# Kernel optimization log

Hardware: AMD Instinct MI355X
Metric: run time of the kernel (lower is better)

## Reference

```python
import jax, jax.numpy as jnp
import numpy as np

TEMPERATURE = 0.05
EPS_NORM = 1e-12  # F.normalize eps
EPS_DEN = 1e-6


def _l2norm_c(x):
    # F.normalize(x, dim=1): x / max(||x||_2, eps)
    n = jnp.sqrt(jnp.sum(x * x, axis=1, keepdims=True))
    return x / jnp.maximum(n, EPS_NORM)


def setup_inputs() -> dict:
    key = jax.random.key(0)
    k1, k2, k3, k4 = jax.random.split(key, 4)
    N, C, H, W = 4, 256, 64, 64
    return {
        "rgb_map": jax.random.normal(k1, (N, C, H, W), dtype=jnp.float32),
        "ir_map": jax.random.normal(k2, (N, C, H, W), dtype=jnp.float32),
        "rgb_mask": jax.random.randint(k3, (N, H, W), 0, 5, dtype=jnp.int64 if jax.config.jax_enable_x64 else jnp.int32),
        "ir_mask": jax.random.randint(k4, (N, H, W), 0, 5, dtype=jnp.int64 if jax.config.jax_enable_x64 else jnp.int32),
    }


def reference(rgb_map, ir_map, rgb_mask, ir_mask):
    N, C, H, W = rgb_map.shape
    HW = H * W
    rgb = _l2norm_c(rgb_map).reshape(N, C, HW)  # (N,C,HW)
    ir = _l2norm_c(ir_map).reshape(N, C, HW)    # (N,C,HW)
    rm = rgb_mask.reshape(N, HW)
    im = ir_mask.reshape(N, HW)

    # pairwise label-equality mask (N, HW, HW)
    mask = (rm[:, :, None] == im[:, None, :]).astype(jnp.float32)
    fg_mask = jnp.concatenate([rm, im], axis=0) > 0  # (2N, HW)

    # cosine similarity matrix, clamped, exponentiated
    logit = jnp.clip(jnp.einsum('ncp,ncq->npq', rgb, ir), -1.0, 1.0)
    e = jnp.exp(logit / TEMPERATURE)  # (N, HW, HW)

    num = e * mask
    r_rgb = num.sum(-1) / (e.sum(-1) + EPS_DEN)  # (N, HW)
    r_ir = num.sum(-2) / (e.sum(-2) + EPS_DEN)   # (N, HW)
    loss = jnp.concatenate([r_rgb, r_ir], axis=0) * fg_mask  # (2N, HW)

    # mean of -log over nonzero entries (faithful to loss[loss != 0])
    nz = loss != 0
    safe = jnp.where(nz, loss, 1.0)
    total = jnp.sum(jnp.where(nz, -jnp.log(safe), 0.0))
    count = jnp.maximum(jnp.sum(nz).astype(jnp.float32), 1.0)
    return total / count
```

## Files before the change

### kernel.cpp

```cpp
#include <hip/hip_runtime.h>
#include <math.h>
#include <stdint.h>

#define NB 4
#define CC 256
#define HWD 4096
#define NPIX (NB * HWD)

typedef __attribute__((ext_vector_type(8))) short bf16x8;
typedef __attribute__((ext_vector_type(4))) float f32x4;

#define VMW8()  asm volatile("s_waitcnt vmcnt(8)" ::: "memory")
#define VMW4()  asm volatile("s_waitcnt vmcnt(4)" ::: "memory")
#define VMW0()  asm volatile("s_waitcnt vmcnt(0)" ::: "memory")
#define LGKM0() asm volatile("s_waitcnt lgkmcnt(0)" ::: "memory")
#define SCHED0() __builtin_amdgcn_sched_barrier(0)
#define SBAR()  __builtin_amdgcn_s_barrier()

__device__ __forceinline__ void gload16(const void* g, void* l) {
    using GP = const __attribute__((address_space(1))) uint32_t*;
    using LP = __attribute__((address_space(3))) uint32_t*;
    __builtin_amdgcn_global_load_lds((GP)g, (LP)l, 16, 0, 0);
}

__device__ __forceinline__ float dpp_rowsum16(float v) {
    v += __int_as_float(__builtin_amdgcn_update_dpp(0, __float_as_int(v), 0x111, 0xf, 0xf, true));
    v += __int_as_float(__builtin_amdgcn_update_dpp(0, __float_as_int(v), 0x112, 0xf, 0xf, true));
    v += __int_as_float(__builtin_amdgcn_update_dpp(0, __float_as_int(v), 0x114, 0xf, 0xf, true));
    v += __int_as_float(__builtin_amdgcn_update_dpp(0, __float_as_int(v), 0x118, 0xf, 0xf, true));
    return v;
}

__global__ __launch_bounds__(512) void normcvt(
    const float* __restrict__ rgb, const float* __restrict__ ir,
    ushort* __restrict__ Abf, ushort* __restrict__ Bbf)
{
    __shared__ float ssbuf[8][64];
    __shared__ float rnl[64];
    const float* src = blockIdx.y ? ir : rgb;
    ushort* dst = blockIdx.y ? Bbf : Abf;
    const int t = threadIdx.x;
    const int p = t & 63, sg = t >> 6;
    const int P = blockIdx.x * 64 + p;
    const int n = P >> 12, pl = P & (HWD - 1);
    const float* base = src + ((size_t)n * CC) * HWD + pl;
    const int c0 = sg * 32;

    float x[32];
    float ss = 0.f;
#pragma unroll
    for (int i = 0; i < 32; ++i) {
        x[i] = base[(size_t)(c0 + i) * HWD];
        ss = fmaf(x[i], x[i], ss);
    }
    ssbuf[sg][p] = ss;
    __syncthreads();
    if (t < 64) {
        float s2 = 0.f;
#pragma unroll
        for (int g = 0; g < 8; ++g) s2 += ssbuf[g][t];
        rnl[t] = 1.0f / fmaxf(sqrtf(s2), 1e-12f);
    }
    __syncthreads();
    const float rn = rnl[p];

    uint pk[16];
#pragma unroll
    for (int i = 0; i < 16; ++i) {
        float x0 = x[2 * i] * rn;
        float x1 = x[2 * i + 1] * rn;
        uint u0 = __float_as_uint(x0); u0 += 0x7fffu + ((u0 >> 16) & 1u);
        uint u1 = __float_as_uint(x1); u1 += 0x7fffu + ((u1 >> 16) & 1u);
        pk[i] = (u0 >> 16) | (u1 & 0xffff0000u);
    }
    uint4* o = (uint4*)(dst + (size_t)P * CC + c0);
#pragma unroll
    for (int k = 0; k < 4; ++k)
        o[k] = make_uint4(pk[4 * k], pk[4 * k + 1], pk[4 * k + 2], pk[4 * k + 3]);
}

__global__ __launch_bounds__(256, 2) void gemm_mfma(
    const ushort* __restrict__ Abf, const ushort* __restrict__ Bbf,
    const int* __restrict__ rmask, const int* __restrict__ imask,
    float2* __restrict__ prow, float2* __restrict__ pcol)
{
    __shared__ __align__(16) ushort As[3][128][32];
    __shared__ __align__(16) ushort Bs[3][128][32];

    const int n  = blockIdx.z;
    const int lin = blockIdx.y * 32 + blockIdx.x;
    const int swz = (lin & 7) * 128 + (lin >> 3);
    const int qt = swz & 31, pt = swz >> 5;
    const int q0 = qt * 128, p0 = pt * 128;

    const int t  = threadIdx.x;
    const int lane = t & 63;
    const int wv = t >> 6, wr = wv >> 1, wc = wv & 1;
    const int kg = lane >> 4, rl = lane & 15;

    const ushort* Ab = Abf + ((size_t)n * HWD + p0) * CC;
    const ushort* Bb = Bbf + ((size_t)n * HWD + q0) * CC;

    const ushort* gA[2]; const ushort* gB[2];
    char* lA[2]; char* lB[2];
#pragma unroll
    for (int it = 0; it < 2; ++it) {
        int slot = it * 256 + t;
        int r = slot >> 2, pos = slot & 3;
        int g = pos ^ ((r >> 1) & 3);
        gA[it] = Ab + (size_t)r * CC + g * 8;
        gB[it] = Bb + (size_t)r * CC + g * 8;
        lA[it] = ((char*)As) + it * 4096 + (t & 192) * 16;
        lB[it] = ((char*)Bs) + it * 4096 + (t & 192) * 16;
    }
#define STAGE(BUFB, C0)                                                        \
    {                                                                          \
        _Pragma("unroll")                                                      \
        for (int it = 0; it < 2; ++it) {                                       \
            gload16(gA[it] + (C0), lA[it] + (BUFB));                           \
            gload16(gB[it] + (C0), lB[it] + (BUFB));                           \
        }                                                                      \
    }

    const ushort* ap[4]; const ushort* bp[4];
#pragma unroll
    for (int mi = 0; mi < 4; ++mi) {
        int r = wr * 64 + mi * 16 + rl;
        ap[mi] = &As[0][r][((kg ^ ((r >> 1) & 3)) * 8)];
    }
#pragma unroll
    for (int ni = 0; ni < 4; ++ni) {
        int r = wc * 64 + ni * 16 + rl;
        bp[ni] = &Bs[0][r][((kg ^ ((r >> 1) & 3)) * 8)];
    }

    f32x4 acc[4][4];
#pragma unroll
    for (int mi = 0; mi < 4; ++mi)
#pragma unroll
        for (int ni = 0; ni < 4; ++ni) acc[mi][ni] = (f32x4){0.f, 0.f, 0.f, 0.f};

    STAGE(0, 0);
    STAGE(8192, 32);
    STAGE(16384, 64);
    SCHED0();

#define KITER(BUF, VMWAIT, RESTAGE)                                            \
    {                                                                          \
        VMWAIT;                                                                \
        SCHED0();                                                              \
        SBAR();                                                                \
        SCHED0();                                                              \
        RESTAGE;                                                               \
        bf16x8 a[4], b[4];                                                     \
        _Pragma("unroll")                                                      \
        for (int mi = 0; mi < 4; ++mi)                                         \
            a[mi] = *(const bf16x8*)(ap[mi] + (BUF) * 4096);                   \
        _Pragma("unroll")                                                      \
        for (int ni = 0; ni < 4; ++ni)                                         \
            b[ni] = *(const bf16x8*)(bp[ni] + (BUF) * 4096);                   \
        LGKM0();                                                               \
        SCHED0();                                                              \
        __builtin_amdgcn_s_setprio(1);                                         \
        _Pragma("unroll")                                                      \
        for (int mi = 0; mi < 4; ++mi)                                         \
            _Pragma("unroll")                                                  \
            for (int ni = 0; ni < 4; ++ni)                                     \
                acc[mi][ni] = __builtin_amdgcn_mfma_f32_16x16x32_bf16(         \
                    a[mi], b[ni], acc[mi][ni], 0, 0, 0);                       \
        __builtin_amdgcn_s_setprio(0);                                         \
        SCHED0();                                                              \
    }

    KITER(0, VMW8(), );
    KITER(1, VMW4(), STAGE(0, 96));
    KITER(2, VMW4(), STAGE(8192, 128));
    KITER(0, VMW4(), STAGE(16384, 160));
    KITER(1, VMW4(), STAGE(0, 192));
    KITER(2, VMW4(), STAGE(8192, 224));
    KITER(0, VMW4(), );
    KITER(1, VMW0(), );
#undef KITER
#undef STAGE

    const int* rmp = rmask + (size_t)n * HWD + p0 + wr * 64;
    const int* imp = imask + (size_t)n * HWD + q0 + wc * 64;
    int clab[4];
#pragma unroll
    for (int ni = 0; ni < 4; ++ni) clab[ni] = imp[ni * 16 + rl];

    float* rb = (float*)As;
    float* cb = rb + 512;

    const float SC = 28.853900817779268f;
    float cn[4] = {0.f, 0.f, 0.f, 0.f}, cd[4] = {0.f, 0.f, 0.f, 0.f};

#pragma unroll
    for (int mi = 0; mi < 4; ++mi) {
        int4 r4 = *(const int4*)(rmp + mi * 16 + kg * 4);
        int rlab[4] = {r4.x, r4.y, r4.z, r4.w};
        float rn4[4] = {0.f, 0.f, 0.f, 0.f}, rd4[4] = {0.f, 0.f, 0.f, 0.f};
#pragma unroll
        for (int ni = 0; ni < 4; ++ni) {
#pragma unroll
            for (int j = 0; j < 4; ++j) {
                float s = fminf(fmaxf(acc[mi][ni][j], -1.f), 1.f);
                float e = exp2f(s * SC);
                rd4[j] += e;
                cd[ni] += e;
                bool m = (rlab[j] == clab[ni]);
                rn4[j] += m ? e : 0.f;
                cn[ni] += m ? e : 0.f;
            }
        }
#pragma unroll
        for (int j = 0; j < 4; ++j) {
            rn4[j] = dpp_rowsum16(rn4[j]);
            rd4[j] = dpp_rowsum16(rd4[j]);
        }
        if (rl == 15) {
            int row = wr * 64 + mi * 16 + kg * 4;
#pragma unroll
            for (int j = 0; j < 4; ++j) {
                rb[(wc * 2 + 0) * 128 + row + j] = rn4[j];
                rb[(wc * 2 + 1) * 128 + row + j] = rd4[j];
            }
        }
    }
#pragma unroll
    for (int ni = 0; ni < 4; ++ni) {
        cn[ni] += __shfl_xor(cn[ni], 16); cn[ni] += __shfl_xor(cn[ni], 32);
        cd[ni] += __shfl_xor(cd[ni], 16); cd[ni] += __shfl_xor(cd[ni], 32);
    }
    if (kg == 0) {
#pragma unroll
        for (int ni = 0; ni < 4; ++ni) {
            int col = wc * 64 + ni * 16 + rl;
            cb[(wr * 2 + 0) * 128 + col] = cn[ni];
            cb[(wr * 2 + 1) * 128 + col] = cd[ni];
        }
    }
    __syncthreads();
    if (t < 128) {
        float2 r2 = make_float2(rb[t] + rb[256 + t], rb[128 + t] + rb[384 + t]);
        prow[(size_t)qt * NPIX + (size_t)n * HWD + p0 + t] = r2;
        float2 c2 = make_float2(cb[t] + cb[256 + t], cb[128 + t] + cb[384 + t]);
        pcol[(size_t)pt * NPIX + (size_t)n * HWD + q0 + t] = c2;
    }
}

__global__ __launch_bounds__(256) void loss_reduce(
    const float2* __restrict__ prow, const float2* __restrict__ pcol,
    const int* __restrict__ rmask, const int* __restrict__ imask,
    float* __restrict__ accum)
{
    __shared__ float sbuf[2][4];
    int idx = blockIdx.x * 256 + threadIdx.x;
    float num = 0.f, den = 0.f; int fg;
    if (idx < NPIX) {
        fg = rmask[idx] > 0;
#pragma unroll 8
        for (int q = 0; q < 32; ++q) {
            float2 v = prow[(size_t)q * NPIX + idx];
            num += v.x; den += v.y;
        }
    } else {
        int k = idx - NPIX;
        fg = imask[k] > 0;
#pragma unroll 8
        for (int p = 0; p < 32; ++p) {
            float2 v = pcol[(size_t)p * NPIX + k];
            num += v.x; den += v.y;
        }
    }
    float v = 0.f, cnt = 0.f;
    if (fg && num > 0.f) {
        float r = num / (den + 1e-6f);
        v = -__logf(r);
        cnt = 1.f;
    }
#pragma unroll
    for (int m = 1; m <= 32; m <<= 1) {
        v += __shfl_xor(v, m);
        cnt += __shfl_xor(cnt, m);
    }
    int lane = threadIdx.x & 63, wave = threadIdx.x >> 6;
    if (lane == 0) { sbuf[0][wave] = v; sbuf[1][wave] = cnt; }
    __syncthreads();
    if (threadIdx.x == 0) {
        atomicAdd(&accum[0], sbuf[0][0] + sbuf[0][1] + sbuf[0][2] + sbuf[0][3]);
        atomicAdd(&accum[1], sbuf[1][0] + sbuf[1][1] + sbuf[1][2] + sbuf[1][3]);
    }
}

__global__ void finalize(const float* __restrict__ accum, float* __restrict__ out) {
    out[0] = accum[0] / fmaxf(accum[1], 1.0f);
}

extern "C" void kernel_launch(void* const* d_in, const int* in_sizes, int n_in,
                              void* d_out, int out_size, void* d_ws, size_t ws_size,
                              hipStream_t stream) {
    const float* rgb = (const float*)d_in[0];
    const float* ir  = (const float*)d_in[1];
    const int* rm = (const int*)d_in[2];
    const int* im = (const int*)d_in[3];
    float* out = (float*)d_out;

    const size_t NE = (size_t)NPIX * CC;
    ushort* Abf = (ushort*)d_ws;
    ushort* Bbf = Abf + NE;
    float2* prow = (float2*)(Bbf + NE);
    float2* pcol = prow + (size_t)32 * NPIX;
    float* accum = (float*)(pcol + (size_t)32 * NPIX);

    hipMemsetAsync(accum, 0, 2 * sizeof(float), stream);

    normcvt<<<dim3(NPIX / 64, 2), 512, 0, stream>>>(rgb, ir, Abf, Bbf);
    gemm_mfma<<<dim3(HWD / 128, HWD / 128, NB), 256, 0, stream>>>(
        Abf, Bbf, rm, im, prow, pcol);
    loss_reduce<<<(2 * NPIX) / 256, 256, 0, stream>>>(prow, pcol, rm, im, accum);
    finalize<<<1, 1, 0, stream>>>(accum, out);
}
```

Measured before the change: 87.98 us.

## Switch similarity GEMM operands from bf16 to fp8 e4m3

The normalisation kernel now packs the normalised features to fp8 instead of bf16, halving the workspace written and later read by the GEMM. The GEMM reworks its LDS tiles, swizzled addressing and staging schedule for byte-sized elements. Each 64-wide K chunk now issues two fp8 16x16x32 MFMAs per tile, so the K loop shrinks from eight iterations to four. The epilogue scratch buffer is moved to a different LDS offset. The trade-off is precision: fp8 rounding of the cosine similarities is amplified by exp(s/0.05), which could push the loss outside tolerance.

```diff
diff --git a/kernel.cpp b/kernel.cpp
--- a/kernel.cpp
+++ b/kernel.cpp
@@ -7,8 +7,8 @@
 #define HWD 4096
 #define NPIX (NB * HWD)
 
-typedef __attribute__((ext_vector_type(8))) short bf16x8;
 typedef __attribute__((ext_vector_type(4))) float f32x4;
+typedef unsigned long long u64;
 
 #define VMW8()  asm volatile("s_waitcnt vmcnt(8)" ::: "memory")
 #define VMW4()  asm volatile("s_waitcnt vmcnt(4)" ::: "memory")
@@ -33,12 +33,12 @@
 
 __global__ __launch_bounds__(512) void normcvt(
     const float* __restrict__ rgb, const float* __restrict__ ir,
-    ushort* __restrict__ Abf, ushort* __restrict__ Bbf)
+    unsigned char* __restrict__ Abf, unsigned char* __restrict__ Bbf)
 {
     __shared__ float ssbuf[8][64];
     __shared__ float rnl[64];
     const float* src = blockIdx.y ? ir : rgb;
-    ushort* dst = blockIdx.y ? Bbf : Abf;
+    unsigned char* dst = blockIdx.y ? Bbf : Abf;
     const int t = threadIdx.x;
     const int p = t & 63, sg = t >> 6;
     const int P = blockIdx.x * 64 + p;
@@ -64,28 +64,25 @@
     __syncthreads();
     const float rn = rnl[p];
 
-    uint pk[16];
-#pragma unroll
-    for (int i = 0; i < 16; ++i) {
-        float x0 = x[2 * i] * rn;
-        float x1 = x[2 * i + 1] * rn;
-        uint u0 = __float_as_uint(x0); u0 += 0x7fffu + ((u0 >> 16) & 1u);
-        uint u1 = __float_as_uint(x1); u1 += 0x7fffu + ((u1 >> 16) & 1u);
-        pk[i] = (u0 >> 16) | (u1 & 0xffff0000u);
+    uint pk[8];
+#pragma unroll
+    for (int i = 0; i < 8; ++i) {
+        int v = __builtin_amdgcn_cvt_pk_fp8_f32(x[4 * i] * rn, x[4 * i + 1] * rn, 0, false);
+        v = __builtin_amdgcn_cvt_pk_fp8_f32(x[4 * i + 2] * rn, x[4 * i + 3] * rn, v, true);
+        pk[i] = (uint)v;
     }
     uint4* o = (uint4*)(dst + (size_t)P * CC + c0);
-#pragma unroll
-    for (int k = 0; k < 4; ++k)
-        o[k] = make_uint4(pk[4 * k], pk[4 * k + 1], pk[4 * k + 2], pk[4 * k + 3]);
+    o[0] = make_uint4(pk[0], pk[1], pk[2], pk[3]);
+    o[1] = make_uint4(pk[4], pk[5], pk[6], pk[7]);
 }
 
 __global__ __launch_bounds__(256, 2) void gemm_mfma(
-    const ushort* __restrict__ Abf, const ushort* __restrict__ Bbf,
+    const unsigned char* __restrict__ Abf, const unsigned char* __restrict__ Bbf,
     const int* __restrict__ rmask, const int* __restrict__ imask,
     float2* __restrict__ prow, float2* __restrict__ pcol)
 {
-    __shared__ __align__(16) ushort As[3][128][32];
-    __shared__ __align__(16) ushort Bs[3][128][32];
+    __shared__ __align__(16) unsigned char As[3][128][64];
+    __shared__ __align__(16) unsigned char Bs[3][128][64];
 
     const int n  = blockIdx.z;
     const int lin = blockIdx.y * 32 + blockIdx.x;
@@ -98,18 +95,18 @@
     const int wv = t >> 6, wr = wv >> 1, wc = wv & 1;
     const int kg = lane >> 4, rl = lane & 15;
 
-    const ushort* Ab = Abf + ((size_t)n * HWD + p0) * CC;
-    const ushort* Bb = Bbf + ((size_t)n * HWD + q0) * CC;
-
-    const ushort* gA[2]; const ushort* gB[2];
+    const unsigned char* Ab = Abf + ((size_t)n * HWD + p0) * CC;
+    const unsigned char* Bb = Bbf + ((size_t)n * HWD + q0) * CC;
+
+    const unsigned char* gA[2]; const unsigned char* gB[2];
     char* lA[2]; char* lB[2];
 #pragma unroll
     for (int it = 0; it < 2; ++it) {
         int slot = it * 256 + t;
         int r = slot >> 2, pos = slot & 3;
         int g = pos ^ ((r >> 1) & 3);
-        gA[it] = Ab + (size_t)r * CC + g * 8;
-        gB[it] = Bb + (size_t)r * CC + g * 8;
+        gA[it] = Ab + (size_t)r * CC + g * 16;
+        gB[it] = Bb + (size_t)r * CC + g * 16;
         lA[it] = ((char*)As) + it * 4096 + (t & 192) * 16;
         lB[it] = ((char*)Bs) + it * 4096 + (t & 192) * 16;
     }
@@ -122,16 +119,18 @@
         }                                                                      \
     }
 
-    const ushort* ap[4]; const ushort* bp[4];
+    const char* ap[4]; const char* bp[4];
 #pragma unroll
     for (int mi = 0; mi < 4; ++mi) {
         int r = wr * 64 + mi * 16 + rl;
-        ap[mi] = &As[0][r][((kg ^ ((r >> 1) & 3)) * 8)];
+        int c16 = (kg >> 1) ^ ((r >> 1) & 3);
+        ap[mi] = ((const char*)As) + r * 64 + c16 * 16 + (kg & 1) * 8;
     }
 #pragma unroll
     for (int ni = 0; ni < 4; ++ni) {
         int r = wc * 64 + ni * 16 + rl;
-        bp[ni] = &Bs[0][r][((kg ^ ((r >> 1) & 3)) * 8)];
+        int c16 = (kg >> 1) ^ ((r >> 1) & 3);
+        bp[ni] = ((const char*)Bs) + r * 64 + c16 * 16 + (kg & 1) * 8;
     }
 
     f32x4 acc[4][4];
@@ -141,24 +140,30 @@
         for (int ni = 0; ni < 4; ++ni) acc[mi][ni] = (f32x4){0.f, 0.f, 0.f, 0.f};
 
     STAGE(0, 0);
-    STAGE(8192, 32);
-    STAGE(16384, 64);
+    STAGE(8192, 64);
+    STAGE(16384, 128);
     SCHED0();
 
-#define KITER(BUF, VMWAIT, RESTAGE)                                            \
+#define KITER(BUFB, VMWAIT, RESTAGE)                                           \
     {                                                                          \
         VMWAIT;                                                                \
         SCHED0();                                                              \
         SBAR();                                                                \
         SCHED0();                                                              \
         RESTAGE;                                                               \
-        bf16x8 a[4], b[4];                                                     \
-        _Pragma("unroll")                                                      \
-        for (int mi = 0; mi < 4; ++mi)                                         \
-            a[mi] = *(const bf16x8*)(ap[mi] + (BUF) * 4096);                   \
-        _Pragma("unroll")                                                      \
-        for (int ni = 0; ni < 4; ++ni)                                         \
-            b[ni] = *(const bf16x8*)(bp[ni] + (BUF) * 4096);                   \
+        u64 a0[4], b0[4], a1[4], b1[4];                                        \
+        _Pragma("unroll")                                                      \
+        for (int mi = 0; mi < 4; ++mi) {                                       \
+            uintptr_t pa = (uintptr_t)(ap[mi] + (BUFB));                       \
+            a0[mi] = *(const u64*)pa;                                          \
+            a1[mi] = *(const u64*)(pa ^ 32);                                   \
+        }                                                                      \
+        _Pragma("unroll")                                                      \
+        for (int ni = 0; ni < 4; ++ni) {                                       \
+            uintptr_t pb = (uintptr_t)(bp[ni] + (BUFB));                       \
+            b0[ni] = *(const u64*)pb;                                          \
+            b1[ni] = *(const u64*)(pb ^ 32);                                   \
+        }                                                                      \
         LGKM0();                                                               \
         SCHED0();                                                              \
         __builtin_amdgcn_s_setprio(1);                                         \
@@ -166,20 +171,22 @@
         for (int mi = 0; mi < 4; ++mi)                                         \
             _Pragma("unroll")                                                  \
             for (int ni = 0; ni < 4; ++ni)                                     \
-                acc[mi][ni] = __builtin_amdgcn_mfma_f32_16x16x32_bf16(         \
-                    a[mi], b[ni], acc[mi][ni], 0, 0, 0);                       \
+                acc[mi][ni] = __builtin_amdgcn_mfma_f32_16x16x32_fp8_fp8(      \
+                    (long)a0[mi], (long)b0[ni], acc[mi][ni], 0, 0, 0);         \
+        _Pragma("unroll")                                                      \
+        for (int mi = 0; mi < 4; ++mi)                                         \
+            _Pragma("unroll")                                                  \
+            for (int ni = 0; ni < 4; ++ni)                                     \
+                acc[mi][ni] = __builtin_amdgcn_mfma_f32_16x16x32_fp8_fp8(      \
+                    (long)a1[mi], (long)b1[ni], acc[mi][ni], 0, 0, 0);         \
         __builtin_amdgcn_s_setprio(0);                                         \
         SCHED0();                                                              \
     }
 
-    KITER(0, VMW8(), );
-    KITER(1, VMW4(), STAGE(0, 96));
-    KITER(2, VMW4(), STAGE(8192, 128));
-    KITER(0, VMW4(), STAGE(16384, 160));
-    KITER(1, VMW4(), STAGE(0, 192));
-    KITER(2, VMW4(), STAGE(8192, 224));
-    KITER(0, VMW4(), );
-    KITER(1, VMW0(), );
+    KITER(0,     VMW8(), );
+    KITER(8192,  VMW4(), STAGE(0, 192));
+    KITER(16384, VMW4(), );
+    KITER(0,     VMW0(), );
 #undef KITER
 #undef STAGE
 
@@ -189,7 +196,7 @@
 #pragma unroll
     for (int ni = 0; ni < 4; ++ni) clab[ni] = imp[ni * 16 + rl];
 
-    float* rb = (float*)As;
+    float* rb = (float*)((char*)As + 16384);
     float* cb = rb + 512;
 
     const float SC = 28.853900817779268f;
@@ -307,8 +314,8 @@
     float* out = (float*)d_out;
 
     const size_t NE = (size_t)NPIX * CC;
-    ushort* Abf = (ushort*)d_ws;
-    ushort* Bbf = Abf + NE;
+    unsigned char* Abf = (unsigned char*)d_ws;
+    unsigned char* Bbf = Abf + NE;
     float2* prow = (float2*)(Bbf + NE);
     float2* pcol = prow + (size_t)32 * NPIX;
     float* accum = (float*)(pcol + (size_t)32 * NPIX);
```

Measured after the change: 78.41 us. 1.12x faster.
